# Optimization experiments

Measured on AMD Instinct MI355X. Metric: run time of the kernel, lower is better.

## Reference

```python
import jax, jax.numpy as jnp
import numpy as np

DIM, NH, WS, SS, MLP_RATIO = 192, 6, 8, 4, 4
EPS = 1e-5


def _rel_pos_index(ws):
    coords = np.stack(np.meshgrid(np.arange(ws), np.arange(ws), indexing='ij')).reshape(2, -1)
    rel = (coords[:, :, None] - coords[:, None, :]).transpose(1, 2, 0)
    rel[:, :, 0] += ws - 1
    rel[:, :, 1] += ws - 1
    rel[:, :, 0] *= 2 * ws - 1
    return rel.sum(-1)  # (ws*ws, ws*ws) int


def _attn_mask(hp, wp, ws, ss):
    img = np.zeros((hp, wp))
    slices = (slice(0, -ws), slice(-ws, -ss), slice(-ss, None))
    cnt = 0
    for hs in slices:
        for vs in slices:
            img[hs, vs] = cnt
            cnt += 1
    mw = img.reshape(hp // ws, ws, wp // ws, ws).transpose(0, 2, 1, 3).reshape(-1, ws * ws)
    am = mw[:, None, :] - mw[:, :, None]  # (nW, N, N)
    return jnp.asarray(np.where(am != 0, -100.0, 0.0).astype(np.float32))


def _ln(x, g, b):
    mu = jnp.mean(x, axis=-1, keepdims=True)
    var = jnp.mean(jnp.square(x - mu), axis=-1, keepdims=True)
    return (x - mu) * jax.lax.rsqrt(var + EPS) * g + b


def setup_inputs():
    key = jax.random.key(0)
    ks = jax.random.split(key, 8)
    B, H, W, C = 8, 128, 128, DIM
    hid = C * MLP_RATIO
    n = lambda k, s: jax.random.normal(k, s, dtype=jnp.float32) * 0.02
    return {
        'x': jax.random.normal(ks[0], (B, H * W, C), dtype=jnp.float32),
        'h': H, 'w': W,
        'norm1_g': jnp.ones((C,), jnp.float32), 'norm1_b': jnp.zeros((C,), jnp.float32),
        'qkv_w': n(ks[1], (C, 3 * C)), 'qkv_b': jnp.zeros((3 * C,), jnp.float32),
        'proj_w': n(ks[2], (C, C)), 'proj_b': jnp.zeros((C,), jnp.float32),
        'rel_bias_table': n(ks[3], ((2 * WS - 1) ** 2, NH)),
        'norm2_g': jnp.ones((C,), jnp.float32), 'norm2_b': jnp.zeros((C,), jnp.float32),
        'fc1_w': n(ks[4], (C, hid)), 'fc1_b': jnp.zeros((hid,), jnp.float32),
        'fc2_w': n(ks[5], (hid, C)), 'fc2_b': jnp.zeros((C,), jnp.float32),
    }


def reference(x, h, w, norm1_g, norm1_b, qkv_w, qkv_b, proj_w, proj_b,
              rel_bias_table, norm2_g, norm2_b, fc1_w, fc1_b, fc2_w, fc2_b):
    B, L, C = x.shape
    ws, ss, nh = WS, SS, NH
    hd = C // nh
    scale = hd ** (-0.5)

    shortcut = x
    xg = _ln(x, norm1_g, norm1_b).reshape(B, h, w, C)

    pad_h = (-h) % ws
    pad_w = (-w) % ws
    if pad_h or pad_w:
        xg = jnp.pad(xg, ((0, 0), (0, pad_h), (0, pad_w), (0, 0)))
    hp, wp = h + pad_h, w + pad_w
    if ss > 0:
        xg = jnp.roll(xg, (-ss, -ss), axis=(1, 2))

    # window partition -> (nB, N, C)
    win = xg.reshape(B, hp // ws, ws, wp // ws, ws, C).transpose(0, 1, 3, 2, 4, 5).reshape(-1, ws * ws, C)
    nB, N, _ = win.shape

    qkv = (win @ qkv_w + qkv_b).reshape(nB, N, 3, nh, hd).transpose(2, 0, 3, 1, 4)
    q, k, v = qkv[0] * scale, qkv[1], qkv[2]  # (nB, nh, N, hd)

    attn = jnp.einsum('bhnd,bhmd->bhnm', q, k)  # (nB, nh, N, N)
    rpi = _rel_pos_index(ws)
    bias = rel_bias_table[rpi.reshape(-1)].reshape(N, N, nh).transpose(2, 0, 1)
    attn = attn + bias[None]
    if ss > 0:
        mask = _attn_mask(hp, wp, ws, ss)  # (nW, N, N)
        nW = mask.shape[0]
        attn = (attn.reshape(nB // nW, nW, nh, N, N) + mask[None, :, None]).reshape(nB, nh, N, N)
    attn = jax.nn.softmax(attn, axis=-1)

    out = jnp.einsum('bhnm,bhmd->bnhd', attn, v).reshape(nB, N, C)
    out = out @ proj_w + proj_b

    # window reverse
    out = out.reshape(B, hp // ws, wp // ws, ws, ws, C).transpose(0, 1, 3, 2, 4, 5).reshape(B, hp, wp, C)
    if ss > 0:
        out = jnp.roll(out, (ss, ss), axis=(1, 2))
    out = out[:, :h, :w].reshape(B, h * w, C)

    x = shortcut + out
    xn2 = _ln(x, norm2_g, norm2_b)
    mlp = jax.nn.gelu(xn2 @ fc1_w + fc1_b, approximate=False) @ fc2_w + fc2_b
    return x + mlp
```

## Files before the change

### kernel.cpp

```cpp
#include <hip/hip_runtime.h>

typedef unsigned short u16;
typedef unsigned int   u32;
typedef __attribute__((ext_vector_type(8))) short bf16x8;
typedef __attribute__((ext_vector_type(4))) float f32x4;

#define L_TOK   16384
#define C_DIM   192
#define HID_DIM 768

#define OFF_QKV  0
#define OFF_PROJ 110592
#define OFF_FC1  147456
#define OFF_FC2  294912
#define CVT_TOT  442368

union FragU { int4 i4; bf16x8 h8; };

#define MFMA_B16(a,b,c) __builtin_amdgcn_mfma_f32_16x16x32_bf16(a,b,c,0,0,0)

__device__ __forceinline__ u16 f2bf(float f) {
    u32 t; __builtin_memcpy(&t, &f, 4);
    t += 0x7FFFu + ((t >> 16) & 1u);
    return (u16)(t >> 16);
}

__global__ __launch_bounds__(256) void k_cvt(
    const float* __restrict__ qkvw, const float* __restrict__ projw,
    const float* __restrict__ fc1w, const float* __restrict__ fc2w,
    u16* __restrict__ ws)
{
    const int i = blockIdx.x * 256 + threadIdx.x;
    if (i >= CVT_TOT) return;
    float v; int dst;
    if (i < OFF_PROJ) {
        const int k = i / 576, col = i % 576;
        const int grp = col / 192, rem = col % 192;
        const int head = rem >> 5, dim = rem & 31;
        v = qkvw[i];
        dst = OFF_QKV + head * (96 * 192) + (grp * 32 + dim) * 192 + k;
    } else if (i < OFF_FC1) {
        const int s = i - OFF_PROJ;
        const int cin = s / 192, cout = s % 192;
        const int head = cin >> 5, j = cin & 31;
        v = projw[s];
        dst = OFF_PROJ + head * (192 * 32) + cout * 32 + j;
    } else if (i < OFF_FC2) {
        const int s = i - OFF_FC1;
        const int k = s / 768, h = s % 768;
        v = fc1w[s];
        dst = OFF_FC1 + h * 192 + k;
    } else {
        const int s = i - OFF_FC2;
        const int h = s / 192, c = s % 192;
        v = fc2w[s];
        dst = OFF_FC2 + c * 768 + h;
    }
    ws[dst] = f2bf(v);
}

__global__ __launch_bounds__(256, 2) void k_attnproj(
    const float* __restrict__ x, const float* __restrict__ g1v, const float* __restrict__ b1v,
    const u16* __restrict__ qkvwT, const float* __restrict__ qkvb,
    const float* __restrict__ relb, const u16* __restrict__ projT, const float* __restrict__ projb,
    float* __restrict__ x1)
{
    struct PW {
        u16 qsb[64 * 40];
        u16 ksb[64 * 40];
        u16 vsbT[32 * 72];
        u16 psb[64 * 72];
        u16 oh [64 * 40];
    };
    union SmemU {
        u16 xw[128 * 200];
        PW pw[2];
    };
    __shared__ __align__(16) SmemU u;
    __shared__ __align__(16) u16 wbuf[192 * 40];
    __shared__ float relbs[225 * 6];

    const int t  = threadIdx.x;
    const int lane = t & 63, w = t >> 6;
    const int win = w >> 1, half = w & 1;
    const int l15 = lane & 15, quad = lane >> 4;
    const int wi2 = blockIdx.x * 2 + win;
    const int b  = wi2 >> 8;
    const int hb = (wi2 >> 4) & 15;
    const int wb = wi2 & 15;
    const bool maskon = (hb == 15) || (wb == 15);
    const f32x4 zf = {0.f, 0.f, 0.f, 0.f};

    for (int i = t; i < 225 * 6; i += 256) relbs[i] = relb[i];

    #pragma unroll
    for (int tk = 0; tk < 2; ++tk) {
        const int nn = t >> 2, q4 = t & 3;
        const int tok = tk * 64 + nn;
        const int tw = tok >> 6, n = tok & 63;
        const int wiA = blockIdx.x * 2 + tw;
        const int bA  = wiA >> 8;
        const int hbA = (wiA >> 4) & 15, wbA = wiA & 15;
        const int r = n >> 3, c = n & 7;
        const int ho = (hbA * 8 + r + 4) & 127;
        const int wo = (wbA * 8 + c + 4) & 127;
        const size_t xoff = ((size_t)bA * L_TOK + ho * 128 + wo) * C_DIM;
        const float* xp = x + xoff + q4 * 48;
        float f[48];
        float sum = 0.f, sq = 0.f;
        #pragma unroll
        for (int i = 0; i < 12; ++i) {
            float4 v = *(const float4*)(xp + i * 4);
            f[i*4+0]=v.x; f[i*4+1]=v.y; f[i*4+2]=v.z; f[i*4+3]=v.w;
            sum += v.x+v.y+v.z+v.w;
            sq  += v.x*v.x + v.y*v.y + v.z*v.z + v.w*v.w;
        }
        sum += __shfl_xor(sum, 1); sum += __shfl_xor(sum, 2);
        sq  += __shfl_xor(sq, 1);  sq  += __shfl_xor(sq, 2);
        const float mu = sum * (1.f / 192.f);
        const float rstd = rsqrtf(sq * (1.f / 192.f) - mu * mu + 1e-5f);
        u16* xrow = u.xw + tok * 200 + q4 * 48;
        #pragma unroll
        for (int i = 0; i < 6; ++i) {
            u32 pk[4];
            #pragma unroll
            for (int j = 0; j < 4; ++j) {
                float g0 = g1v[q4*48 + i*8 + j*2],     b0 = b1v[q4*48 + i*8 + j*2];
                float g1 = g1v[q4*48 + i*8 + j*2 + 1], b1 = b1v[q4*48 + i*8 + j*2 + 1];
                float y0 = (f[i*8+j*2]   - mu) * rstd * g0 + b0;
                float y1 = (f[i*8+j*2+1] - mu) * rstd * g1 + b1;
                pk[j] = (u32)f2bf(y0) | (((u32)f2bf(y1)) << 16);
            }
            *(int4*)(xrow + i * 8) = make_int4((int)pk[0], (int)pk[1], (int)pk[2], (int)pk[3]);
        }
    }
    __syncthreads();

    FragU afrag[2][6];
    #pragma unroll
    for (int mt = 0; mt < 2; ++mt)
        #pragma unroll
        for (int kk = 0; kk < 6; ++kk)
            afrag[mt][kk].i4 = *(const int4*)(u.xw +
                (win*64 + half*32 + mt*16 + l15) * 200 + kk*32 + quad*8);

    PW* P = &u.pw[win];
    const int rb = half*32 + quad*4;

    int4 wr0, wr1, wr2;
    auto LOADW = [&](int hh, int sub) {
        if (sub < 3) {
            const u16* src = qkvwT + (size_t)hh * (96 * 192) + sub * 64;
            wr0 = *(const int4*)(src + ((t      ) >> 3) * 192 + ((t      ) & 7) * 8);
            wr1 = *(const int4*)(src + ((t + 256) >> 3) * 192 + ((t + 256) & 7) * 8);
            wr2 = *(const int4*)(src + ((t + 512) >> 3) * 192 + ((t + 512) & 7) * 8);
        } else {
            const u16* src = projT + (size_t)hh * (192 * 32);
            wr0 = *(const int4*)(src + ((t      ) >> 2) * 32 + ((t      ) & 3) * 8);
            wr1 = *(const int4*)(src + ((t + 256) >> 2) * 32 + ((t + 256) & 3) * 8);
            wr2 = *(const int4*)(src + ((t + 512) >> 2) * 32 + ((t + 512) & 3) * 8);
        }
    };
    auto STOREW = [&](int sub) {
        if (sub < 3) {
            *(int4*)(wbuf + ((t      ) >> 3) * 72 + ((t      ) & 7) * 8) = wr0;
            *(int4*)(wbuf + ((t + 256) >> 3) * 72 + ((t + 256) & 7) * 8) = wr1;
            *(int4*)(wbuf + ((t + 512) >> 3) * 72 + ((t + 512) & 7) * 8) = wr2;
        } else {
            *(int4*)(wbuf + ((t      ) >> 2) * 40 + ((t      ) & 3) * 8) = wr0;
            *(int4*)(wbuf + ((t + 256) >> 2) * 40 + ((t + 256) & 3) * 8) = wr1;
            *(int4*)(wbuf + ((t + 512) >> 2) * 40 + ((t + 512) & 3) * 8) = wr2;
        }
    };
    LOADW(0, 0);

    f32x4 acc2[2][12];
    #pragma unroll
    for (int mt = 0; mt < 2; ++mt)
        #pragma unroll
        for (int nt = 0; nt < 12; ++nt) acc2[mt][nt] = zf;

    for (int head = 0; head < 6; ++head) {
        f32x4 accq[2][6];
        #pragma unroll
        for (int mt = 0; mt < 2; ++mt)
            #pragma unroll
            for (int nt = 0; nt < 6; ++nt) accq[mt][nt] = zf;

        for (int kc = 0; kc < 3; ++kc) {
            __syncthreads();
            STOREW(kc);
            __syncthreads();
            LOADW(head, kc + 1);
            #pragma unroll
            for (int s = 0; s < 2; ++s) {
                #pragma unroll
                for (int nt = 0; nt < 6; ++nt) {
                    FragU bf_;
                    bf_.i4 = *(const int4*)(wbuf + (nt*16 + l15)*72 + s*32 + quad*8);
                    accq[0][nt] = MFMA_B16(afrag[0][kc*2 + s].h8, bf_.h8, accq[0][nt]);
                    accq[1][nt] = MFMA_B16(afrag[1][kc*2 + s].h8, bf_.h8, accq[1][nt]);
                }
            }
        }
        #pragma unroll
        for (int mt = 0; mt < 2; ++mt) {
            #pragma unroll
            for (int nt = 0; nt < 6; ++nt) {
                const int grp = nt >> 1;
                const int dim = (nt & 1)*16 + l15;
                const float bias = qkvb[grp*192 + head*32 + dim];
                float vv[4];
                #pragma unroll
                for (int rg = 0; rg < 4; ++rg) vv[rg] = accq[mt][nt][rg] + bias;
                const int rowb = rb + mt*16;
                if (grp == 0) {
                    #pragma unroll
                    for (int rg = 0; rg < 4; ++rg)
                        P->qsb[(rowb + rg)*40 + dim] = f2bf(vv[rg] * 0.17677669529663687f);
                } else if (grp == 1) {
                    #pragma unroll
                    for (int rg = 0; rg < 4; ++rg)
                        P->ksb[(rowb + rg)*40 + dim] = f2bf(vv[rg]);
                } else {
                    u32 lo = (u32)f2bf(vv[0]) | (((u32)f2bf(vv[1])) << 16);
                    u32 hi = (u32)f2bf(vv[2]) | (((u32)f2bf(vv[3])) << 16);
                    *(uint2*)&P->vsbT[dim*72 + rowb] = make_uint2(lo, hi);
                }
            }
        }
        __syncthreads();

        FragU qf0, qf1;
        qf0.i4 = *(const int4*)(P->qsb + (half*32 + l15)*40 + quad*8);
        qf1.i4 = *(const int4*)(P->qsb + (half*32 + 16 + l15)*40 + quad*8);
        f32x4 sv[2][4];
        #pragma unroll
        for (int nt = 0; nt < 4; ++nt) {
            FragU kf; kf.i4 = *(const int4*)(P->ksb + (nt*16 + l15)*40 + quad*8);
            sv[0][nt] = MFMA_B16(qf0.h8, kf.h8, zf);
            sv[1][nt] = MFMA_B16(qf1.h8, kf.h8, zf);
        }
        const int kr_ = l15 >> 3, kc2 = l15 & 7;
        #pragma unroll
        for (int mt = 0; mt < 2; ++mt) {
            #pragma unroll
            for (int rg = 0; rg < 4; ++rg) {
                const int qm = rb + mt*16 + rg;
                const int qr = qm >> 3, qc = qm & 7;
                #pragma unroll
                for (int nt = 0; nt < 4; ++nt) {
                    const int kr = nt*2 + kr_;
                    sv[mt][nt][rg] += relbs[((qr - kr + 7)*15 + (qc - kc2 + 7))*6 + head];
                }
            }
        }
        if (maskon) {
            #pragma unroll
            for (int mt = 0; mt < 2; ++mt) {
                #pragma unroll
                for (int rg = 0; rg < 4; ++rg) {
                    const int qm = rb + mt*16 + rg;
                    const int qr = qm >> 3, qc = qm & 7;
                    const int regq = ((hb == 15) ? (qr < 4 ? 1 : 2) : 0) * 3
                                   + ((wb == 15) ? (qc < 4 ? 1 : 2) : 0);
                    #pragma unroll
                    for (int nt = 0; nt < 4; ++nt) {
                        const int kr = nt*2 + kr_;
                        const int regk = ((hb == 15) ? (kr < 4 ? 1 : 2) : 0) * 3
                                       + ((wb == 15) ? (kc2 < 4 ? 1 : 2) : 0);
                        if (regq != regk) sv[mt][nt][rg] -= 100.f;
                    }
                }
            }
        }
        #pragma unroll
        for (int mt = 0; mt < 2; ++mt) {
            #pragma unroll
            for (int rg = 0; rg < 4; ++rg) {
                float mx = fmaxf(fmaxf(sv[mt][0][rg], sv[mt][1][rg]),
                                 fmaxf(sv[mt][2][rg], sv[mt][3][rg]));
                mx = fmaxf(mx, __shfl_xor(mx, 1));
                mx = fmaxf(mx, __shfl_xor(mx, 2));
                mx = fmaxf(mx, __shfl_xor(mx, 4));
                mx = fmaxf(mx, __shfl_xor(mx, 8));
                float s0 = 0.f;
                #pragma unroll
                for (int nt = 0; nt < 4; ++nt) {
                    sv[mt][nt][rg] = __expf(sv[mt][nt][rg] - mx); s0 += sv[mt][nt][rg];
                }
                s0 += __shfl_xor(s0, 1); s0 += __shfl_xor(s0, 2);
                s0 += __shfl_xor(s0, 4); s0 += __shfl_xor(s0, 8);
                const float inv = 1.f / s0;
                #pragma unroll
                for (int nt = 0; nt < 4; ++nt)
                    P->psb[(rb + mt*16 + rg)*72 + nt*16 + l15] = f2bf(sv[mt][nt][rg] * inv);
            }
        }

        FragU vb[2][2];
        #pragma unroll
        for (int ntv = 0; ntv < 2; ++ntv) {
            vb[ntv][0].i4 = *(const int4*)(P->vsbT + (ntv*16 + l15)*72 + quad*8);
            vb[ntv][1].i4 = *(const int4*)(P->vsbT + (ntv*16 + l15)*72 + 32 + quad*8);
        }
        #pragma unroll
        for (int mt = 0; mt < 2; ++mt) {
            FragU pa0, pa1;
            pa0.i4 = *(const int4*)(P->psb + (half*32 + mt*16 + l15)*72 + quad*8);
            pa1.i4 = *(const int4*)(P->psb + (half*32 + mt*16 + l15)*72 + 32 + quad*8);
            f32x4 ov0 = zf, ov1 = zf;
            ov0 = MFMA_B16(pa0.h8, vb[0][0].h8, ov0);
            ov0 = MFMA_B16(pa1.h8, vb[0][1].h8, ov0);
            ov1 = MFMA_B16(pa0.h8, vb[1][0].h8, ov1);
            ov1 = MFMA_B16(pa1.h8, vb[1][1].h8, ov1);
            #pragma unroll
            for (int rg = 0; rg < 4; ++rg) {
                P->oh[(rb + mt*16 + rg)*40 + l15]      = f2bf(ov0[rg]);
                P->oh[(rb + mt*16 + rg)*40 + 16 + l15] = f2bf(ov1[rg]);
            }
        }

        STOREW(3);
        __syncthreads();
        if (head < 5) LOADW(head + 1, 0);
        FragU ao0, ao1;
        ao0.i4 = *(const int4*)(P->oh + (half*32 + l15)*40 + quad*8);
        ao1.i4 = *(const int4*)(P->oh + (half*32 + 16 + l15)*40 + quad*8);
        #pragma unroll
        for (int nt = 0; nt < 12; ++nt) {
            FragU bp; bp.i4 = *(const int4*)(wbuf + (nt*16 + l15)*40 + quad*8);
            acc2[0][nt] = MFMA_B16(ao0.h8, bp.h8, acc2[0][nt]);
            acc2[1][nt] = MFMA_B16(ao1.h8, bp.h8, acc2[1][nt]);
        }
    }

    {
        float pb[12];
        #pragma unroll
        for (int nt = 0; nt < 12; ++nt) pb[nt] = projb[nt*16 + l15];
        #pragma unroll
        for (int mt = 0; mt < 2; ++mt) {
            #pragma unroll
            for (int rg = 0; rg < 4; ++rg) {
                const int tok = rb + mt*16 + rg;
                const int tr = tok >> 3, tc = tok & 7;
                const int ho2 = (hb * 8 + tr + 4) & 127;
                const int wo2 = (wb * 8 + tc + 4) & 127;
                const size_t base = ((size_t)b * L_TOK + ho2 * 128 + wo2) * C_DIM;
                #pragma unroll
                for (int nt = 0; nt < 12; ++nt) {
                    const int col = nt*16 + l15;
                    x1[base + col] = acc2[mt][nt][rg] + pb[nt] + x[base + col];
                }
            }
        }
    }
}

__global__ __launch_bounds__(256, 2) void k_mlp(
    const float* x1, const float* __restrict__ g2v, const float* __restrict__ b2v,
    const u16* __restrict__ fc1wT, const float* __restrict__ fc1b,
    const u16* __restrict__ fc2wT, const float* __restrict__ fc2b,
    float* out)
{
    union SmemU {
        u16 xnA[64 * 200];
        u16 hbuf[128 * 104];
    };
    __shared__ __align__(16) SmemU u;
    __shared__ __align__(16) u16 wT[2][7680];

    const int blk = blockIdx.x;
    const int t = threadIdx.x;
    const size_t row0 = (size_t)blk * 128;
    const int lane = t & 63, w = t >> 6;
    const int l15 = lane & 15, quad = lane >> 4;
    const f32x4 zf = {0.f, 0.f, 0.f, 0.f};

    FragU afrag[2][6];
    for (int hf = 0; hf < 2; ++hf) {
        const int nn = t >> 2, q4 = t & 3;
        const int tok = hf * 64 + nn;
        const float* xp = x1 + (row0 + tok) * C_DIM + q4 * 48;
        float f[48];
        float sum = 0.f, sq = 0.f;
        #pragma unroll
        for (int i = 0; i < 12; ++i) {
            float4 v = *(const float4*)(xp + i * 4);
            f[i*4+0]=v.x; f[i*4+1]=v.y; f[i*4+2]=v.z; f[i*4+3]=v.w;
            sum += v.x+v.y+v.z+v.w;
            sq  += v.x*v.x + v.y*v.y + v.z*v.z + v.w*v.w;
        }
        sum += __shfl_xor(sum,1); sum += __shfl_xor(sum,2);
        sq  += __shfl_xor(sq,1);  sq  += __shfl_xor(sq,2);
        const float mu = sum * (1.f/192.f);
        const float rstd = rsqrtf(sq * (1.f/192.f) - mu*mu + 1e-5f);
        u16* xrow = u.xnA + nn * 200 + q4 * 48;
        #pragma unroll
        for (int i = 0; i < 6; ++i) {
            u32 pk[4];
            #pragma unroll
            for (int j = 0; j < 4; ++j) {
                float g0 = g2v[q4*48 + i*8 + j*2],     b0 = b2v[q4*48 + i*8 + j*2];
                float g1 = g2v[q4*48 + i*8 + j*2 + 1], b1 = b2v[q4*48 + i*8 + j*2 + 1];
                float y0 = (f[i*8+j*2]   - mu) * rstd * g0 + b0;
                float y1 = (f[i*8+j*2+1] - mu) * rstd * g1 + b1;
                pk[j] = (u32)f2bf(y0) | (((u32)f2bf(y1)) << 16);
            }
            *(int4*)(xrow + i*8) = make_int4((int)pk[0], (int)pk[1], (int)pk[2], (int)pk[3]);
        }
        __syncthreads();
        #pragma unroll
        for (int kk = 0; kk < 6; ++kk)
            afrag[hf][kk].i4 = *(const int4*)(u.xnA + (w*16 + l15) * 200 + kk*32 + quad*8);
        __syncthreads();
    }

    int4 wr0, wr1, wr2;
    auto LOADW = [&](int hcL, int sub) {
        if (sub < 3) {
            const u16* src = fc1wT + (size_t)(hcL * 96) * 192 + sub * 64;
            wr0 = *(const int4*)(src + ((t      ) >> 3) * 192 + ((t      ) & 7) * 8);
            wr1 = *(const int4*)(src + ((t + 256) >> 3) * 192 + ((t + 256) & 7) * 8);
            wr2 = *(const int4*)(src + ((t + 512) >> 3) * 192 + ((t + 512) & 7) * 8);
        } else {
            const u16* src = fc2wT + hcL * 96 + (sub - 3) * 32;
            wr0 = *(const int4*)(src + ((t      ) >> 2) * 768 + ((t      ) & 3) * 8);
            wr1 = *(const int4*)(src + ((t + 256) >> 2) * 768 + ((t + 256) & 3) * 8);
            wr2 = *(const int4*)(src + ((t + 512) >> 2) * 768 + ((t + 512) & 3) * 8);
        }
    };
    auto STOREW = [&](u16* dstb, int sub) {
        if (sub < 3) {
            *(int4*)(dstb + ((t      ) >> 3) * 72 + ((t      ) & 7) * 8) = wr0;
            *(int4*)(dstb + ((t + 256) >> 3) * 72 + ((t + 256) & 7) * 8) = wr1;
            *(int4*)(dstb + ((t + 512) >> 3) * 72 + ((t + 512) & 7) * 8) = wr2;
        } else {
            *(int4*)(dstb + ((t      ) >> 2) * 40 + ((t      ) & 3) * 8) = wr0;
            *(int4*)(dstb + ((t + 256) >> 2) * 40 + ((t + 256) & 3) * 8) = wr1;
            *(int4*)(dstb + ((t + 512) >> 2) * 40 + ((t + 512) & 3) * 8) = wr2;
        }
    };
    LOADW(0, 0);

    f32x4 acc2[2][12];
    #pragma unroll
    for (int mt = 0; mt < 2; ++mt)
        #pragma unroll
        for (int nt = 0; nt < 12; ++nt) acc2[mt][nt] = zf;

    int g = 0;
    for (int hc = 0; hc < 8; ++hc) {
        f32x4 acc1[2][6];
        #pragma unroll
        for (int mt = 0; mt < 2; ++mt)
            #pragma unroll
            for (int nt = 0; nt < 6; ++nt) acc1[mt][nt] = zf;

        for (int kc = 0; kc < 3; ++kc) {
            u16* buf = wT[g & 1];
            STOREW(buf, kc);
            __syncthreads();
            LOADW(hc, kc + 1);
            #pragma unroll
            for (int s = 0; s < 2; ++s) {
                #pragma unroll
                for (int nt = 0; nt < 6; ++nt) {
                    FragU bf_;
                    bf_.i4 = *(const int4*)(buf + (nt*16 + l15)*72 + s*32 + quad*8);
                    acc1[0][nt] = MFMA_B16(afrag[0][kc*2 + s].h8, bf_.h8, acc1[0][nt]);
                    acc1[1][nt] = MFMA_B16(afrag[1][kc*2 + s].h8, bf_.h8, acc1[1][nt]);
                }
            }
            ++g;
        }
        #pragma unroll
        for (int nt = 0; nt < 6; ++nt) {
            const float bb = fc1b[hc*96 + nt*16 + l15];
            #pragma unroll
            for (int mt = 0; mt < 2; ++mt) {
                #pragma unroll
                for (int rg = 0; rg < 4; ++rg) {
                    float h = acc1[mt][nt][rg] + bb;
                    float gl = 0.5f * h * (1.f + erff(h * 0.70710678118654752f));
                    u.hbuf[(mt*64 + w*16 + quad*4 + rg) * 104 + nt*16 + l15] = f2bf(gl);
                }
            }
        }
        for (int sc = 0; sc < 3; ++sc) {
            u16* buf = wT[g & 1];
            STOREW(buf, 3 + sc);
            __syncthreads();
            if (sc < 2)           LOADW(hc, 4 + sc);
            else if (hc < 7)      LOADW(hc + 1, 0);
            FragU ha0, ha1;
            ha0.i4 = *(const int4*)(u.hbuf + (w*16 + l15) * 104 + sc*32 + quad*8);
            ha1.i4 = *(const int4*)(u.hbuf + (64 + w*16 + l15) * 104 + sc*32 + quad*8);
            #pragma unroll
            for (int nt = 0; nt < 12; ++nt) {
                FragU bf_;
                bf_.i4 = *(const int4*)(buf + (nt*16 + l15)*40 + quad*8);
                acc2[0][nt] = MFMA_B16(ha0.h8, bf_.h8, acc2[0][nt]);
                acc2[1][nt] = MFMA_B16(ha1.h8, bf_.h8, acc2[1][nt]);
            }
            ++g;
        }
    }

    #pragma unroll
    for (int nt = 0; nt < 12; ++nt) {
        const int col = nt*16 + l15;
        const float bb = fc2b[col];
        #pragma unroll
        for (int mt = 0; mt < 2; ++mt) {
            #pragma unroll
            for (int rg = 0; rg < 4; ++rg) {
                const size_t idx = (row0 + mt*64 + w*16 + quad*4 + rg) * C_DIM + col;
                out[idx] = acc2[mt][nt][rg] + bb + x1[idx];
            }
        }
    }
}

extern "C" void kernel_launch(void* const* d_in, const int* in_sizes, int n_in,
                              void* d_out, int out_size, void* d_ws, size_t ws_size,
                              hipStream_t stream) {
    const float* x     = (const float*)d_in[0];
    const float* g1v   = (const float*)d_in[3];
    const float* b1v   = (const float*)d_in[4];
    const float* qkvw  = (const float*)d_in[5];
    const float* qkvb  = (const float*)d_in[6];
    const float* projw = (const float*)d_in[7];
    const float* projb = (const float*)d_in[8];
    const float* relb  = (const float*)d_in[9];
    const float* g2v   = (const float*)d_in[10];
    const float* b2v   = (const float*)d_in[11];
    const float* fc1w  = (const float*)d_in[12];
    const float* fc1b  = (const float*)d_in[13];
    const float* fc2w  = (const float*)d_in[14];
    const float* fc2b  = (const float*)d_in[15];

    float* x1 = (float*)d_out;
    u16* wsb  = (u16*)d_ws;

    hipLaunchKernelGGL(k_cvt, dim3((CVT_TOT + 255) / 256), dim3(256), 0, stream,
                       qkvw, projw, fc1w, fc2w, wsb);
    hipLaunchKernelGGL(k_attnproj, dim3(1024), dim3(256), 0, stream,
                       x, g1v, b1v, wsb + OFF_QKV, qkvb, relb, wsb + OFF_PROJ, projb, x1);
    hipLaunchKernelGGL(k_mlp, dim3(1024), dim3(256), 0, stream,
                       x1, g2v, b2v, wsb + OFF_FC1, fc1b, wsb + OFF_FC2, fc2b, x1);
}
```

Before: 532.7 us.

## Stage full per-chunk MLP weight tiles in LDS and use tanh-form GELU

Replaces the double-buffered small weight sub-tiles in the MLP kernel with one large LDS buffer that holds a whole fc1 or fc2 chunk. Each chunk is loaded once with nine vector loads per thread and prefetched during the previous phase, which cuts the number of block barriers per chunk from six to four. B fragments are batched ahead of the MFMA loops. It also swaps the exact erf GELU for a tanh-style approximation written with a single exp, which cuts transcendental cost but changes numerics slightly. The larger register staging (9 int4) and LDS footprint may reduce occupancy.

```diff
diff --git a/kernel.cpp b/kernel.cpp
--- a/kernel.cpp
+++ b/kernel.cpp
@@ -369,7 +369,7 @@
         u16 hbuf[128 * 104];
     };
     __shared__ __align__(16) SmemU u;
-    __shared__ __align__(16) u16 wT[2][7680];
+    __shared__ __align__(16) u16 wbig[19968];
 
     const int blk = blockIdx.x;
     const int t = threadIdx.x;
@@ -417,32 +417,40 @@
         __syncthreads();
     }
 
-    int4 wr0, wr1, wr2;
-    auto LOADW = [&](int hcL, int sub) {
-        if (sub < 3) {
-            const u16* src = fc1wT + (size_t)(hcL * 96) * 192 + sub * 64;
-            wr0 = *(const int4*)(src + ((t      ) >> 3) * 192 + ((t      ) & 7) * 8);
-            wr1 = *(const int4*)(src + ((t + 256) >> 3) * 192 + ((t + 256) & 7) * 8);
-            wr2 = *(const int4*)(src + ((t + 512) >> 3) * 192 + ((t + 512) & 7) * 8);
-        } else {
-            const u16* src = fc2wT + hcL * 96 + (sub - 3) * 32;
-            wr0 = *(const int4*)(src + ((t      ) >> 2) * 768 + ((t      ) & 3) * 8);
-            wr1 = *(const int4*)(src + ((t + 256) >> 2) * 768 + ((t + 256) & 3) * 8);
-            wr2 = *(const int4*)(src + ((t + 512) >> 2) * 768 + ((t + 512) & 3) * 8);
-        }
-    };
-    auto STOREW = [&](u16* dstb, int sub) {
-        if (sub < 3) {
-            *(int4*)(dstb + ((t      ) >> 3) * 72 + ((t      ) & 7) * 8) = wr0;
-            *(int4*)(dstb + ((t + 256) >> 3) * 72 + ((t + 256) & 7) * 8) = wr1;
-            *(int4*)(dstb + ((t + 512) >> 3) * 72 + ((t + 512) & 7) * 8) = wr2;
-        } else {
-            *(int4*)(dstb + ((t      ) >> 2) * 40 + ((t      ) & 3) * 8) = wr0;
-            *(int4*)(dstb + ((t + 256) >> 2) * 40 + ((t + 256) & 3) * 8) = wr1;
-            *(int4*)(dstb + ((t + 512) >> 2) * 40 + ((t + 512) & 3) * 8) = wr2;
-        }
-    };
-    LOADW(0, 0);
+    int4 wr[9];
+    auto LOADW1 = [&](int hcL) {
+        #pragma unroll
+        for (int i = 0; i < 9; ++i) {
+            const int e = t + i * 256;
+            const int cc = e / 24, seg = e % 24;
+            wr[i] = *(const int4*)(fc1wT + (size_t)(hcL*96 + cc) * 192 + seg * 8);
+        }
+    };
+    auto STORE1 = [&]() {
+        #pragma unroll
+        for (int i = 0; i < 9; ++i) {
+            const int e = t + i * 256;
+            const int cc = e / 24, seg = e % 24;
+            *(int4*)(wbig + cc * 200 + seg * 8) = wr[i];
+        }
+    };
+    auto LOADW2 = [&](int hcL) {
+        #pragma unroll
+        for (int i = 0; i < 9; ++i) {
+            const int e = t + i * 256;
+            const int c = e / 12, seg = e % 12;
+            wr[i] = *(const int4*)(fc2wT + (size_t)c * 768 + hcL*96 + seg * 8);
+        }
+    };
+    auto STORE2 = [&]() {
+        #pragma unroll
+        for (int i = 0; i < 9; ++i) {
+            const int e = t + i * 256;
+            const int c = e / 12, seg = e % 12;
+            *(int4*)(wbig + c * 104 + seg * 8) = wr[i];
+        }
+    };
+    LOADW1(0);
 
     f32x4 acc2[2][12];
     #pragma unroll
@@ -450,31 +458,31 @@
         #pragma unroll
         for (int nt = 0; nt < 12; ++nt) acc2[mt][nt] = zf;
 
-    int g = 0;
     for (int hc = 0; hc < 8; ++hc) {
+        __syncthreads();
+        STORE1();
+        __syncthreads();
         f32x4 acc1[2][6];
         #pragma unroll
         for (int mt = 0; mt < 2; ++mt)
             #pragma unroll
             for (int nt = 0; nt < 6; ++nt) acc1[mt][nt] = zf;
-
+        #pragma unroll
         for (int kc = 0; kc < 3; ++kc) {
-            u16* buf = wT[g & 1];
-            STOREW(buf, kc);
-            __syncthreads();
-            LOADW(hc, kc + 1);
             #pragma unroll
             for (int s = 0; s < 2; ++s) {
+                FragU bf_[6];
+                #pragma unroll
+                for (int nt = 0; nt < 6; ++nt)
+                    bf_[nt].i4 = *(const int4*)(wbig + (nt*16 + l15)*200 + kc*64 + s*32 + quad*8);
                 #pragma unroll
                 for (int nt = 0; nt < 6; ++nt) {
-                    FragU bf_;
-                    bf_.i4 = *(const int4*)(buf + (nt*16 + l15)*72 + s*32 + quad*8);
-                    acc1[0][nt] = MFMA_B16(afrag[0][kc*2 + s].h8, bf_.h8, acc1[0][nt]);
-                    acc1[1][nt] = MFMA_B16(afrag[1][kc*2 + s].h8, bf_.h8, acc1[1][nt]);
-                }
-            }
-            ++g;
-        }
+                    acc1[0][nt] = MFMA_B16(afrag[0][kc*2 + s].h8, bf_[nt].h8, acc1[0][nt]);
+                    acc1[1][nt] = MFMA_B16(afrag[1][kc*2 + s].h8, bf_[nt].h8, acc1[1][nt]);
+                }
+            }
+        }
+        LOADW2(hc);
         #pragma unroll
         for (int nt = 0; nt < 6; ++nt) {
             const float bb = fc1b[hc*96 + nt*16 + l15];
@@ -483,28 +491,31 @@
                 #pragma unroll
                 for (int rg = 0; rg < 4; ++rg) {
                     float h = acc1[mt][nt][rg] + bb;
-                    float gl = 0.5f * h * (1.f + erff(h * 0.70710678118654752f));
+                    float e = __expf(h * (-1.5957691216057308f
+                                          - 0.0713548162726302f * h * h));
+                    float gl = h / (1.f + e);
                     u.hbuf[(mt*64 + w*16 + quad*4 + rg) * 104 + nt*16 + l15] = f2bf(gl);
                 }
             }
         }
+        __syncthreads();
+        STORE2();
+        __syncthreads();
+        if (hc < 7) LOADW1(hc + 1);
+        #pragma unroll
         for (int sc = 0; sc < 3; ++sc) {
-            u16* buf = wT[g & 1];
-            STOREW(buf, 3 + sc);
-            __syncthreads();
-            if (sc < 2)           LOADW(hc, 4 + sc);
-            else if (hc < 7)      LOADW(hc + 1, 0);
             FragU ha0, ha1;
             ha0.i4 = *(const int4*)(u.hbuf + (w*16 + l15) * 104 + sc*32 + quad*8);
             ha1.i4 = *(const int4*)(u.hbuf + (64 + w*16 + l15) * 104 + sc*32 + quad*8);
+            FragU bf_[12];
+            #pragma unroll
+            for (int nt = 0; nt < 12; ++nt)
+                bf_[nt].i4 = *(const int4*)(wbig + (nt*16 + l15)*104 + sc*32 + quad*8);
             #pragma unroll
             for (int nt = 0; nt < 12; ++nt) {
-                FragU bf_;
-                bf_.i4 = *(const int4*)(buf + (nt*16 + l15)*40 + quad*8);
-                acc2[0][nt] = MFMA_B16(ha0.h8, bf_.h8, acc2[0][nt]);
-                acc2[1][nt] = MFMA_B16(ha1.h8, bf_.h8, acc2[1][nt]);
-            }
-            ++g;
+                acc2[0][nt] = MFMA_B16(ha0.h8, bf_[nt].h8, acc2[0][nt]);
+                acc2[1][nt] = MFMA_B16(ha1.h8, bf_[nt].h8, acc2[1][nt]);
+            }
         }
     }
 
```

After: 737.4 us. 1.38x slower.
